# Kernel optimization log

Measured on AMD Instinct MI355X. Metric: run time of the kernel, lower is better.

The kernel has to match this reference:

```python
import jax, jax.numpy as jnp
import numpy as np

MAX_DIST = 35.0
GRID_RES = 1.0
BOX = int(np.ceil(2 * MAX_DIST / GRID_RES + 1))  # 71


def setup_inputs() -> dict:
    key = jax.random.key(0)
    k1, k2 = jax.random.split(key)
    B, N, F = 8, 16384, 32
    # spread ~N(0, 20): most points inside [-35, 35] box, some outside (mask path)
    coords = jax.random.normal(k1, (B, N, 3), dtype=jnp.float32) * 20.0
    features = jax.random.normal(k2, (B, N, F), dtype=jnp.float32)
    return {"coords": coords, "features": features}


def reference(coords, features):
    B, N, _ = coords.shape
    F = features.shape[2]
    # quantize coords to integer grid cells
    gc = jnp.round((coords + MAX_DIST) / GRID_RES).astype(jnp.int32)  # [B,N,3]
    in_box = jnp.all((gc >= 0) & (gc < BOX), axis=2)                  # [B,N]
    # jit-friendly equivalent of boolean_mask+scatter_nd: zero out-of-box
    # updates and clamp their indices (adding zero is a no-op).
    gc_c = jnp.clip(gc, 0, BOX - 1)
    upd = jnp.where(in_box[..., None], features, 0.0)                 # [B,N,F]
    grid = jnp.zeros((B, BOX, BOX, BOX, F), dtype=features.dtype)
    # FAITHFUL to original: batch index column is tf.zeros -> every point
    # scatters (with duplicate-index summation) into batch slice 0.
    grid = grid.at[0, gc_c[..., 0], gc_c[..., 1], gc_c[..., 2]].add(upd)
    return grid
```

## Files before the change

kernel.cpp:

```cpp
#include <hip/hip_runtime.h>

#define BOX 71
#define NF 32
#define MAX_DIST_F 35.0f

__global__ __launch_bounds__(256) void MakeGrid_scatter_kernel(
    const float* __restrict__ coords,
    const float* __restrict__ features,
    float* __restrict__ grid,
    int total_points)
{
    int t = blockIdx.x * blockDim.x + threadIdx.x;
    int p = t >> 5;
    int f = t & 31;
    if (p >= total_points) return;

    float cx = coords[p * 3 + 0];
    float cy = coords[p * 3 + 1];
    float cz = coords[p * 3 + 2];

    float rx = rintf(cx + MAX_DIST_F);
    float ry = rintf(cy + MAX_DIST_F);
    float rz = rintf(cz + MAX_DIST_F);
    int gx = (int)rx;
    int gy = (int)ry;
    int gz = (int)rz;

    bool in_box = (gx >= 0) & (gx < BOX) &
                  (gy >= 0) & (gy < BOX) &
                  (gz >= 0) & (gz < BOX);
    if (!in_box) return;

    float v = features[(size_t)p * NF + f];
    size_t idx = (((size_t)gx * BOX + gy) * BOX + gz) * NF + f;
    atomicAdd(grid + idx, v);
}

extern "C" void kernel_launch(void* const* d_in, const int* in_sizes, int n_in,
                              void* d_out, int out_size, void* d_ws, size_t ws_size,
                              hipStream_t stream) {
    const float* coords   = (const float*)d_in[0];
    const float* features = (const float*)d_in[1];
    float* out = (float*)d_out;

    hipMemsetAsync(out, 0, (size_t)out_size, stream);

    int total_points = in_sizes[0] / 3;
    int total_threads = total_points * NF;
    int blocks = (total_threads + 255) / 256;
    MakeGrid_scatter_kernel<<<blocks, 256, 0, stream>>>(coords, features, out, total_points);
}
```

Before: 328.7 us.

## Fuse zeroing of untouched batch slices into scatter kernel to overlap work

```diff
diff --git a/kernel.cpp b/kernel.cpp
--- a/kernel.cpp
+++ b/kernel.cpp
@@ -4,36 +4,50 @@
 #define NF 32
 #define MAX_DIST_F 35.0f
 
-__global__ __launch_bounds__(256) void MakeGrid_scatter_kernel(
+#define SLICE_FLOATS (BOX * BOX * BOX * NF)
+#define SLICE_BYTES  ((size_t)SLICE_FLOATS * 4)
+#define REST_F4      ((7 * SLICE_FLOATS) / 4)
+
+typedef float f32x4 __attribute__((ext_vector_type(4)));
+
+__global__ __launch_bounds__(256) void fused_zero_scatter(
     const float* __restrict__ coords,
     const float* __restrict__ features,
     float* __restrict__ grid,
-    int total_points)
+    int total_points,
+    int nzb)
 {
-    int t = blockIdx.x * blockDim.x + threadIdx.x;
-    int p = t >> 5;
-    int f = t & 31;
-    if (p >= total_points) return;
+    if (blockIdx.x % 5 == 0) {
+        int zid = blockIdx.x / 5;
+        f32x4* rest = (f32x4*)(grid + SLICE_FLOATS);
+        const f32x4 z = {0.f, 0.f, 0.f, 0.f};
+        int stride = nzb * 256;
+        for (int i = zid * 256 + (int)threadIdx.x; i < REST_F4; i += stride)
+            rest[i] = z;
+    } else {
+        int sid = blockIdx.x - 1 - blockIdx.x / 5;
+        int t = sid * 256 + (int)threadIdx.x;
+        int p = t >> 5;
+        int f = t & 31;
+        if (p >= total_points) return;
 
-    float cx = coords[p * 3 + 0];
-    float cy = coords[p * 3 + 1];
-    float cz = coords[p * 3 + 2];
+        float cx = coords[p * 3 + 0];
+        float cy = coords[p * 3 + 1];
+        float cz = coords[p * 3 + 2];
 
-    float rx = rintf(cx + MAX_DIST_F);
-    float ry = rintf(cy + MAX_DIST_F);
-    float rz = rintf(cz + MAX_DIST_F);
-    int gx = (int)rx;
-    int gy = (int)ry;
-    int gz = (int)rz;
+        int gx = (int)rintf(cx + MAX_DIST_F);
+        int gy = (int)rintf(cy + MAX_DIST_F);
+        int gz = (int)rintf(cz + MAX_DIST_F);
 
-    bool in_box = (gx >= 0) & (gx < BOX) &
-                  (gy >= 0) & (gy < BOX) &
-                  (gz >= 0) & (gz < BOX);
-    if (!in_box) return;
+        bool in_box = (gx >= 0) & (gx < BOX) &
+                      (gy >= 0) & (gy < BOX) &
+                      (gz >= 0) & (gz < BOX);
+        if (!in_box) return;
 
-    float v = features[(size_t)p * NF + f];
-    size_t idx = (((size_t)gx * BOX + gy) * BOX + gz) * NF + f;
-    atomicAdd(grid + idx, v);
+        float v = features[(size_t)p * NF + f];
+        size_t idx = (((size_t)gx * BOX + gy) * BOX + gz) * NF + f;
+        atomicAdd(grid + idx, v);
+    }
 }
 
 extern "C" void kernel_launch(void* const* d_in, const int* in_sizes, int n_in,
@@ -43,10 +57,12 @@
     const float* features = (const float*)d_in[1];
     float* out = (float*)d_out;
 
-    hipMemsetAsync(out, 0, (size_t)out_size, stream);
+    hipMemsetAsync(out, 0, SLICE_BYTES, stream);
 
-    int total_points = in_sizes[0] / 3;
-    int total_threads = total_points * NF;
-    int blocks = (total_threads + 255) / 256;
-    MakeGrid_scatter_kernel<<<blocks, 256, 0, stream>>>(coords, features, out, total_points);
+    int total_points   = in_sizes[0] / 3;
+    int scatter_blocks = (total_points * NF + 255) / 256;
+    int nzb            = 4096;
+    int total_blocks   = scatter_blocks + nzb;
+    fused_zero_scatter<<<total_blocks, 256, 0, stream>>>(
+        coords, features, out, total_points, nzb);
 }
```

Measured after the change: 383.3 us. 1.17x slower.
